# Kernel optimization log

Hardware: AMD Instinct MI355X
Metric: run time of the kernel (lower is better)

The kernel has to match this reference:

```python
import jax, jax.numpy as jnp
import numpy as np
from jax import lax

TOP_K = 2

def _unfold(x_img, k):
    # F.unfold(kernel=k, stride=k): [B,C,H,W] -> [B, C*k*k, L], column index c*k*k + kh*k + kw
    B, C, H, W = x_img.shape
    Hp, Wp = H // k, W // k
    u = x_img.reshape(B, C, Hp, k, Wp, k).transpose(0, 1, 3, 5, 2, 4)
    return u.reshape(B, C * k * k, Hp * Wp)

def _fold(p, k, H, W):
    # F.fold inverse of non-overlapping unfold: [B, C*k*k, L] -> [B,C,H,W]
    B = p.shape[0]
    C = p.shape[1] // (k * k)
    Hp, Wp = H // k, W // k
    u = p.reshape(B, C, k, k, Hp, Wp).transpose(0, 1, 4, 2, 5, 3)
    return u.reshape(B, C, H, W)

def setup_inputs() -> dict:
    key = jax.random.key(0)
    ks = jax.random.split(key, 6)
    B, H, W, C, F, E, P = 8, 64, 64, 384, 1536, 8, 4
    N = H * W
    x = jax.random.normal(ks[0], (B, N, C), dtype=jnp.float32)
    gate_w = jax.random.normal(ks[1], (E, C, P, P), dtype=jnp.float32) * 0.01
    w1 = jax.random.normal(ks[2], (E, C, F), dtype=jnp.float32) * (1.0 / np.sqrt(C))
    b1 = jax.random.normal(ks[3], (E, F), dtype=jnp.float32) * 0.01
    w2 = jax.random.normal(ks[4], (E, F, C), dtype=jnp.float32) * (1.0 / np.sqrt(F))
    b2 = jax.random.normal(ks[5], (E, C), dtype=jnp.float32) * 0.01
    return {"x": x, "gate_w": gate_w, "w1": w1, "b1": b1, "w2": w2, "b2": b2, "H": H, "W": W}

def reference(x, gate_w, w1, b1, w2, b2, H, W):
    B, N, C = x.shape
    E, _, P, _ = gate_w.shape
    k2 = P * P
    Hp, Wp = H // P, W // P
    L = Hp * Wp
    x_img = jnp.transpose(x, (0, 2, 1)).reshape(B, C, H, W)
    # router: strided conv -> logits per patch
    logits_map = lax.conv_general_dilated(
        x_img, gate_w, window_strides=(P, P), padding='VALID',
        dimension_numbers=('NCHW', 'OIHW', 'NCHW'))  # [B,E,Hp,Wp]
    router_logits = jnp.transpose(logits_map, (0, 2, 3, 1)).reshape(B, L, E)
    probs = jax.nn.softmax(router_logits, axis=-1)
    ew, ei = lax.top_k(probs, TOP_K)  # [B,L,topk]
    ew = ew / (jnp.sum(ew, axis=-1, keepdims=True) + 1e-9)
    # expand to token level (faithful to original's reshape/flatten ordering)
    ei_tok = jnp.broadcast_to(ei[:, :, None, :], (B, L, k2, TOP_K)).reshape(-1, TOP_K)
    ew_tok = jnp.broadcast_to(ew[:, :, None, :], (B, L, k2, TOP_K)).reshape(-1, TOP_K)
    # unfold + the original's (scrambled) reshape(B, C, L, k2)
    U = _unfold(x_img, P)  # [B, C*k2, L]
    x_patches = jnp.transpose(U.reshape(B, C, L, k2), (0, 2, 3, 1))  # [B,L,k2,C]
    flat_x = x_patches.reshape(-1, C)  # [T,C], T = B*L*k2
    # combine weights: zero for experts not in top-k == masked dispatch math
    cw = jnp.zeros((flat_x.shape[0], E), dtype=flat_x.dtype)
    for kk in range(TOP_K):
        cw = cw + jax.nn.one_hot(ei_tok[:, kk], E, dtype=flat_x.dtype) * ew_tok[:, kk:kk + 1]
    out = jnp.zeros_like(flat_x)
    for e in range(E):
        h = jax.nn.gelu(flat_x @ w1[e] + b1[e], approximate=False)
        y = h @ w2[e] + b2[e]
        out = out + cw[:, e:e + 1] * y
    # fold back (mirrors original's reshape/permute exactly)
    o = jnp.transpose(out.reshape(B, L, k2, C), (0, 3, 1, 2)).reshape(B, C * k2, L)
    out_img = _fold(o, P, H, W)  # [B,C,H,W]
    # original: output.transpose(1,2).reshape(B,N,C) on NCHW tensor
    output = jnp.transpose(out_img, (0, 2, 1, 3)).reshape(B, N, C)
    return output
```

## Files before the change

kernel.cpp:

```cpp
#include <hip/hip_runtime.h>
#include <hip/hip_bf16.h>

#define BB   8
#define HH   64
#define WWID 64
#define CC   384
#define FF   1536
#define EE   8
#define LL   256
#define MTOTMAX 67584
#define NTMAX   264

typedef unsigned short ushort_t;
typedef __attribute__((ext_vector_type(4))) unsigned short u16x4;
typedef __attribute__((ext_vector_type(8))) short          s16x8;
typedef __attribute__((ext_vector_type(4))) float          f32x4;

__device__ __forceinline__ float bf2f(ushort_t u) {
  union { unsigned int i; float f; } v; v.i = ((unsigned int)u) << 16; return v.f;
}
__device__ __forceinline__ ushort_t f2bf(float f) {
  union { float f; unsigned int i; } v; v.f = f;
  unsigned int u = v.i;
  u += 0x7fffu + ((u >> 16) & 1u);
  return (ushort_t)(u >> 16);
}
__device__ __forceinline__ float gelu_f(float x) {
  float x2 = x * x;
  float t  = __builtin_fmaf(x2, -0.10294325f, -2.3022082f);
  float e  = __builtin_amdgcn_exp2f(x * t);
  float r  = __builtin_amdgcn_rcpf(1.0f + e);
  return x * r;
}

#define GLDS(g, l) __builtin_amdgcn_global_load_lds( \
    (const __attribute__((address_space(1))) void*)(g), \
    (__attribute__((address_space(3))) void*)(l), 16, 0, 0)

__global__ __launch_bounds__(256) void k_transpose(const float* __restrict__ src,
                                                   ushort_t* __restrict__ dst,
                                                   int R, int Cd) {
  __shared__ ushort_t tile[32][33];
  int e  = blockIdx.z;
  int c0 = blockIdx.x * 32, r0 = blockIdx.y * 32;
  int tx = threadIdx.x & 31, ty = threadIdx.x >> 5;
  const float* s = src + (size_t)e * R * Cd;
  ushort_t*    d = dst + (size_t)e * R * Cd;
  #pragma unroll
  for (int i = 0; i < 32; i += 8)
    tile[ty + i][tx] = f2bf(s[(size_t)(r0 + ty + i) * Cd + c0 + tx]);
  __syncthreads();
  #pragma unroll
  for (int i = 0; i < 32; i += 8)
    d[(size_t)(c0 + ty + i) * R + r0 + tx] = tile[tx][ty + i];
}

__global__ void k_tgw(const float* __restrict__ gw, float* __restrict__ gwt) {
  int e = blockIdx.x, t = threadIdx.x;
  for (int i = t; i < CC * 16; i += 256) {
    int c = i >> 4, p = i & 15;
    gwt[((size_t)e * 16 + p) * CC + c] = gw[(size_t)e * CC * 16 + i];
  }
}

__global__ __launch_bounds__(256) void k_router(const float* __restrict__ x,
                                                const float* __restrict__ gwt,
                                                int* __restrict__ re, float* __restrict__ rw,
                                                int* __restrict__ cnt) {
  int bid = blockIdx.x;
  int b = bid >> 8, l2 = bid & 255;
  int hp = l2 >> 4, wp = l2 & 15;
  int t = threadIdx.x;
  int e = t >> 5, lane = t & 31;
  const float* xb = x + (size_t)b * (HH * WWID) * CC;
  const float* ge = gwt + (size_t)e * 16 * CC;
  float acc = 0.f;
  #pragma unroll
  for (int p = 0; p < 16; ++p) {
    int pix = (hp * 4 + (p >> 2)) * 64 + wp * 4 + (p & 3);
    const float* xr = xb + (size_t)pix * CC;
    const float* gr = ge + (size_t)p * CC;
    #pragma unroll
    for (int it = 0; it < 3; ++it) {
      f32x4 xv = *reinterpret_cast<const f32x4*>(xr + it * 128 + lane * 4);
      f32x4 gv = *reinterpret_cast<const f32x4*>(gr + it * 128 + lane * 4);
      acc += xv.x * gv.x + xv.y * gv.y + xv.z * gv.z + xv.w * gv.w;
    }
  }
  #pragma unroll
  for (int d = 16; d; d >>= 1) acc += __shfl_down(acc, d, 32);
  __shared__ float logits[EE];
  if (lane == 0) logits[e] = acc;
  __syncthreads();
  if (t == 0) {
    float m = logits[0];
    #pragma unroll
    for (int i = 1; i < EE; ++i) m = fmaxf(m, logits[i]);
    float p[EE]; float s = 0.f;
    #pragma unroll
    for (int i = 0; i < EE; ++i) { p[i] = __expf(logits[i] - m); s += p[i]; }
    #pragma unroll
    for (int i = 0; i < EE; ++i) p[i] /= s;
    int e0 = 0;
    #pragma unroll
    for (int i = 1; i < EE; ++i) if (p[i] > p[e0]) e0 = i;
    int e1 = (e0 == 0) ? 1 : 0;
    #pragma unroll
    for (int i = 0; i < EE; ++i) if (i != e0 && p[i] > p[e1]) e1 = i;
    float s2 = p[e0] + p[e1] + 1e-9f;
    re[bid * 2 + 0] = e0;  re[bid * 2 + 1] = e1;
    rw[bid * 2 + 0] = p[e0] / s2;  rw[bid * 2 + 1] = p[e1] / s2;
    atomicAdd(&cnt[e0], 16);
    atomicAdd(&cnt[e1], 16);
  }
}

__global__ void k_pad(const int* __restrict__ cnt, int* __restrict__ cntp,
                      int* __restrict__ basep, int* __restrict__ tile2e,
                      int* __restrict__ gids, float* __restrict__ gwts) {
  __shared__ int s_cnt[EE], s_cntp[EE], s_base[EE + 1];
  int t = threadIdx.x;
  if (t == 0) {
    int b = 0;
    for (int e = 0; e < EE; ++e) {
      int c  = cnt[e];
      int cp = (c + 255) & ~255;
      s_cnt[e] = c; s_cntp[e] = cp; s_base[e] = b;
      b += cp;
    }
    s_base[EE] = b;
  }
  __syncthreads();
  if (t < EE) { cntp[t] = s_cntp[t]; basep[t] = s_base[t]; }
  if (t == EE) basep[EE] = s_base[EE];
  int ntot = s_base[EE] >> 8;
  for (int g = t; g < ntot; g += 256) {
    int e = 0;
    #pragma unroll
    for (int i = 1; i < EE; ++i) if (g * 256 >= s_base[i]) e = i;
    tile2e[g] = e;
  }
  for (int e = 0; e < EE; ++e)
    for (int i = s_cnt[e] + t; i < s_cntp[e]; i += 256) {
      gids[s_base[e] + i] = -1;
      gwts[s_base[e] + i] = 0.f;
    }
}

__global__ void k_assign(const int* __restrict__ re, const float* __restrict__ rw,
                         const int* __restrict__ basep, int* __restrict__ cnt2,
                         int* __restrict__ gids, float* __restrict__ gwts,
                         int* __restrict__ inv) {
  int i = blockIdx.x * blockDim.x + threadIdx.x;
  if (i >= BB * LL * 2) return;
  int pat = i >> 1, slot = i & 1;
  int b = pat >> 8, l2 = pat & 255;
  int e = re[i];
  float w = rw[i];
  int t2 = l2 >> 4, hp = l2 & 15;
  int kh = t2 >> 2, kw = t2 & 3;
  int h = hp * 4 + kh;
  int row = basep[e] + atomicAdd(&cnt2[e], 16);
  #pragma unroll
  for (int j = 0; j < 16; ++j) {
    int wpix = j * 4 + kw;
    int pix = (b << 12) + (h << 6) + wpix;
    gids[row + j] = pix;
    gwts[row + j] = w;
    inv[(slot << 15) + pix] = row + j;
  }
}

__global__ __launch_bounds__(256) void k_gather(const float* __restrict__ x,
                                                const int* __restrict__ gids,
                                                const int* __restrict__ basep,
                                                ushort_t* __restrict__ Xc, int t0) {
  int g = t0 + blockIdx.x;
  if (g * 128 >= basep[EE]) return;
  __shared__ int s_id[128];
  int t = threadIdx.x;
  if (t < 128) s_id[t] = gids[g * 128 + t];
  __syncthreads();
  ushort_t* dst = Xc + (size_t)blockIdx.x * 128 * CC;
  for (int i = t; i < 128 * 96; i += 256) {
    int row = i / 96, ch = (i % 96) * 4;
    int id = s_id[row];
    f32x4 v = (f32x4){0.f, 0.f, 0.f, 0.f};
    if (id >= 0) v = *reinterpret_cast<const f32x4*>(x + (size_t)(id & 32767) * CC + ch);
    u16x4 o = {f2bf(v.x), f2bf(v.y), f2bf(v.z), f2bf(v.w)};
    *reinterpret_cast<u16x4*>(dst + (size_t)row * CC + ch) = o;
  }
}

#define STAGE(DST, KOFF)                                                      \
  { _Pragma("unroll")                                                         \
    for (int c = 0; c < NC; ++c)                                              \
      GLDS(src_c[c] + (KOFF), (DST) + (w * NC + c) * 512); }

#define PHASE(VMFULL, RD, DOST, KOFF)                                         \
  {                                                                           \
    if (VMFULL) {                                                             \
      if constexpr (NC == 4) { asm volatile("s_waitcnt vmcnt(4)" ::: "memory"); } \
      else                   { asm volatile("s_waitcnt vmcnt(3)" ::: "memory"); } \
    } else {                                                                  \
      asm volatile("s_waitcnt vmcnt(0)" ::: "memory");                        \
    }                                                                         \
    __builtin_amdgcn_s_barrier();                                             \
    __builtin_amdgcn_sched_barrier(0);                                        \
    s16x8 af[FI], bf[4];                                                      \
    _Pragma("unroll")                                                         \
    for (int i = 0; i < FI; ++i)                                              \
      af[i] = *reinterpret_cast<const s16x8*>((RD) + (wf * FI + i) * 512 + lane * 8); \
    _Pragma("unroll")                                                         \
    for (int j = 0; j < 4; ++j)                                               \
      bf[j] = *reinterpret_cast<const s16x8*>((RD) + (2 * FI + wm * 4 + j) * 512 + lane * 8); \
    asm volatile("s_waitcnt lgkmcnt(0)" ::: "memory");                        \
    __builtin_amdgcn_sched_barrier(0);                                        \
    __builtin_amdgcn_s_barrier();                                             \
    if (DOST) STAGE(RD, KOFF);                                                \
    __builtin_amdgcn_s_setprio(1);                                            \
    _Pragma("unroll")                                                         \
    for (int i = 0; i < FI; ++i)                                              \
      _Pragma("unroll")                                                       \
      for (int j = 0; j < 4; ++j)                                             \
        acc[i][j] = __builtin_amdgcn_mfma_f32_16x16x32_bf16(af[i], bf[j], acc[i][j], 0, 0, 0); \
    __builtin_amdgcn_s_setprio(0);                                            \
  }

template<int K, int NOUT, int TN, bool GELU, bool OUTG>
__global__ __launch_bounds__(512, 2) void k_gemm(const ushort_t* __restrict__ A,
                                                 const ushort_t* __restrict__ Bsrc,
                                                 const float* __restrict__ bias,
                                                 const int* __restrict__ basep,
                                                 const int* __restrict__ tile2e,
                                                 const float* __restrict__ gwts,
                                                 ushort_t* __restrict__ out, int t0) {
  constexpr int FI  = TN / 32;
  constexpr int NCH = 2 * FI + 16;
  constexpr int NC  = NCH / 8;
  constexpr int NX  = NOUT / TN;
  int nwg = NX * (int)gridDim.y;
  int wg  = (int)blockIdx.y * NX + (int)blockIdx.x;
  int id  = ((nwg & 7) == 0) ? ((wg & 7) * (nwg >> 3) + (wg >> 3)) : wg;
  int ng  = id % NX;
  int ly  = id / NX;
  int g   = t0 + ly;
  if (g * 256 >= basep[EE]) return;
  int e = tile2e[g];
  __shared__ ushort_t S[2][NCH * 512];
  int t = threadIdx.x, w = t >> 6, lane = t & 63;
  int l15 = lane & 15, q = lane >> 4;
  int wf = w & 1, wm = w >> 1;
  const ushort_t* a_src = A + ((size_t)e * NOUT + ng * TN) * K;
  const ushort_t* b_src = Bsrc + (size_t)ly * 256 * K;

  const ushort_t* src_c[NC];
  #pragma unroll
  for (int c = 0; c < NC; ++c) {
    int ch = w * NC + c;
    src_c[c] = (ch < 2 * FI)
      ? a_src + (size_t)(ch * 16 + l15) * K + q * 8
      : b_src + (size_t)((ch - 2 * FI) * 16 + l15) * K + q * 8;
  }

  f32x4 acc[FI][4];
  #pragma unroll
  for (int i = 0; i < FI; ++i)
    #pragma unroll
    for (int j = 0; j < 4; ++j) acc[i][j] = (f32x4){0.f, 0.f, 0.f, 0.f};

  ushort_t* S0 = &S[0][0];
  ushort_t* S1 = &S[1][0];

  STAGE(S0, 0);
  STAGE(S1, 32);

  constexpr int NIT = K / 32;
  for (int it = 0; it < NIT - 2; it += 2) {
    PHASE(true, S0, true, (size_t)(it + 2) * 32);
    PHASE(true, S1, true, (size_t)(it + 3) * 32);
  }
  PHASE(true,  S0, false, 0);
  PHASE(false, S1, false, 0);

  int nb = ng * TN + wf * (TN / 2) + q * 4;
  f32x4 bv[FI];
  #pragma unroll
  for (int i = 0; i < FI; ++i)
    bv[i] = *reinterpret_cast<const f32x4*>(bias + (size_t)e * NOUT + nb + i * 16);
  ushort_t* ob = out + (OUTG ? (size_t)g : (size_t)ly) * 256 * NOUT;
  #pragma unroll
  for (int j = 0; j < 4; ++j) {
    int m = wm * 64 + j * 16 + l15;
    float wt = GELU ? 1.f : gwts[g * 256 + m];
    ushort_t* op = ob + (size_t)m * NOUT + nb;
    #pragma unroll
    for (int i = 0; i < FI; ++i) {
      u16x4 v;
      #pragma unroll
      for (int r = 0; r < 4; ++r) {
        float xv = acc[i][j][r] + bv[i][r];
        v[r] = f2bf(GELU ? gelu_f(xv) : xv * wt);
      }
      *reinterpret_cast<u16x4*>(op + i * 16) = v;
    }
  }
}

__global__ __launch_bounds__(256) void k_final(const ushort_t* __restrict__ y,
                                               const int* __restrict__ inv,
                                               float* __restrict__ out) {
  int bid = blockIdx.x;
  __shared__ float tile[64][193];
  __shared__ int s_r0[64], s_r1[64];
  int t = threadIdx.x;
  if (t < 64) {
    s_r0[t] = inv[(bid << 6) + t];
    s_r1[t] = inv[32768 + (bid << 6) + t];
  }
  __syncthreads();
  float* dst = out + (size_t)bid * CC * WWID;
  #pragma unroll
  for (int half = 0; half < 2; ++half) {
    int c0 = half * 192;
    for (int i = t; i < 64 * 48; i += 256) {
      int w = i / 48, c4 = (i % 48) * 4;
      u16x4 a = *reinterpret_cast<const u16x4*>(y + (size_t)s_r0[w] * CC + c0 + c4);
      u16x4 b = *reinterpret_cast<const u16x4*>(y + (size_t)s_r1[w] * CC + c0 + c4);
      #pragma unroll
      for (int k = 0; k < 4; ++k)
        tile[w][c4 + k] = bf2f(a[k]) + bf2f(b[k]);
    }
    __syncthreads();
    for (int i = t; i < 64 * 192; i += 256) {
      int cl = i / 64, w = i % 64;
      dst[(size_t)(c0 + cl) * WWID + w] = tile[w][cl];
    }
    __syncthreads();
  }
}

extern "C" void kernel_launch(void* const* d_in, const int* in_sizes, int n_in,
                              void* d_out, int out_size, void* d_ws, size_t ws_size,
                              hipStream_t stream) {
  const float* x  = (const float*)d_in[0];
  const float* gw = (const float*)d_in[1];
  const float* w1 = (const float*)d_in[2];
  const float* b1 = (const float*)d_in[3];
  const float* w2 = (const float*)d_in[4];
  const float* b2 = (const float*)d_in[5];

  const size_t fixed = (size_t)EE * FF * CC * 2 * 2
                     + (size_t)MTOTMAX * CC * 2
                     + (size_t)EE * 16 * CC * 4
                     + (size_t)MTOTMAX * 4 * 2
                     + (size_t)65536 * 4
                     + (size_t)BB * LL * 2 * 4 * 2
                     + (size_t)NTMAX * 4
                     + 1024;
  const int cands[6] = {32768, 16384, 8192, 4096, 2048, 1024};
  int MC = 1024;
  for (int i = 0; i < 6; ++i)
    if (fixed + (size_t)cands[i] * 3840 <= ws_size) { MC = cands[i]; break; }
  const int npass = (MTOTMAX + MC - 1) / MC;
  const int nt128 = MC / 128;
  const int nt256 = MC / 256;

  char* ws = (char*)d_ws;
  size_t off = 0;
  ushort_t* Xc   = (ushort_t*)(ws + off); off += (size_t)MC * CC * 2;
  ushort_t* Hc   = (ushort_t*)(ws + off); off += (size_t)MC * FF * 2;
  ushort_t* w1t  = (ushort_t*)(ws + off); off += (size_t)EE * FF * CC * 2;
  ushort_t* w2t  = (ushort_t*)(ws + off); off += (size_t)EE * FF * CC * 2;
  ushort_t* y    = (ushort_t*)(ws + off); off += (size_t)MTOTMAX * CC * 2;
  float* gwt   = (float*)(ws + off); off += (size_t)EE * 16 * CC * 4;
  int*   gids  = (int*)(ws + off);   off += (size_t)MTOTMAX * 4;
  float* gwts  = (float*)(ws + off); off += (size_t)MTOTMAX * 4;
  int*   inv   = (int*)(ws + off);   off += (size_t)65536 * 4;
  int*   re    = (int*)(ws + off);   off += (size_t)BB * LL * 2 * 4;
  float* rw    = (float*)(ws + off); off += (size_t)BB * LL * 2 * 4;
  int*   tile2e= (int*)(ws + off);   off += (size_t)NTMAX * 4;
  int*   cnt   = (int*)(ws + off);   off += 64;
  int*   cnt2  = (int*)(ws + off);   off += 64;
  int*   cntp  = (int*)(ws + off);   off += 64;
  int*   basep = (int*)(ws + off);   off += 64;

  hipMemsetAsync(cnt, 0, 128, stream);

  k_transpose<<<dim3(FF / 32, CC / 32, EE), 256, 0, stream>>>(w1, w1t, CC, FF);
  k_transpose<<<dim3(CC / 32, FF / 32, EE), 256, 0, stream>>>(w2, w2t, FF, CC);
  k_tgw<<<EE, 256, 0, stream>>>(gw, gwt);
  k_router<<<BB * LL, 256, 0, stream>>>(x, gwt, re, rw, cnt);
  k_pad<<<1, 256, 0, stream>>>(cnt, cntp, basep, tile2e, gids, gwts);
  k_assign<<<16, 256, 0, stream>>>(re, rw, basep, cnt2, gids, gwts, inv);

  for (int p = 0; p < npass; ++p) {
    k_gather<<<nt128, 256, 0, stream>>>(x, gids, basep, Xc, p * nt128);
    k_gemm<CC, FF, 256, true,  false><<<dim3(FF / 256, nt256), 512, 0, stream>>>(
        w1t, Xc, b1, basep, tile2e, (const float*)nullptr, Hc, p * nt256);
    k_gemm<FF, CC, 128, false, true ><<<dim3(CC / 128, nt256), 512, 0, stream>>>(
        w2t, Hc, b2, basep, tile2e, gwts, y, p * nt256);
  }
  k_final<<<BB * HH, 256, 0, stream>>>(y, inv, (float*)d_out);
}
```

Before: 655.1 us.

## Switch MoE GEMMs to 192x192 tiles with 4 waves and triple-buffered LDS

Both expert GEMMs move from 256-row tiles (256xTN with 8 waves) to 192x192 tiles computed by 4 waves. Each wave now holds a 6x6 MFMA accumulator block, and a three-stage LDS ring replaces the double buffer. Expert token padding drops from multiples of 256 to multiples of 192, which cuts wasted padded rows, and the larger per-wave tile raises MFMA work per LDS read. The cost is heavy register pressure from 36 f32x4 accumulators, 72KB of dynamic LDS per block, and the loss of the XCD-swizzle divisibility for some grid shapes. Pass chunk sizes and workspace constants are rescaled to match.

Measured after the change: 592.9 us. -9.5%, faster.

```diff
diff --git a/kernel.cpp b/kernel.cpp
--- a/kernel.cpp
+++ b/kernel.cpp
@@ -8,8 +8,8 @@
 #define FF   1536
 #define EE   8
 #define LL   256
-#define MTOTMAX 67584
-#define NTMAX   264
+#define MTOTMAX 67200
+#define NTMAX   352
 
 typedef unsigned short ushort_t;
 typedef __attribute__((ext_vector_type(4))) unsigned short u16x4;
@@ -124,7 +124,7 @@
     int b = 0;
     for (int e = 0; e < EE; ++e) {
       int c  = cnt[e];
-      int cp = (c + 255) & ~255;
+      int cp = ((c + 191) / 192) * 192;
       s_cnt[e] = c; s_cntp[e] = cp; s_base[e] = b;
       b += cp;
     }
@@ -133,11 +133,11 @@
   __syncthreads();
   if (t < EE) { cntp[t] = s_cntp[t]; basep[t] = s_base[t]; }
   if (t == EE) basep[EE] = s_base[EE];
-  int ntot = s_base[EE] >> 8;
+  int ntot = s_base[EE] / 192;
   for (int g = t; g < ntot; g += 256) {
     int e = 0;
     #pragma unroll
-    for (int i = 1; i < EE; ++i) if (g * 256 >= s_base[i]) e = i;
+    for (int i = 1; i < EE; ++i) if (g * 192 >= s_base[i]) e = i;
     tile2e[g] = e;
   }
   for (int e = 0; e < EE; ++e)
@@ -194,108 +194,104 @@
 
 #define STAGE(DST, KOFF)                                                      \
   { _Pragma("unroll")                                                         \
-    for (int c = 0; c < NC; ++c)                                              \
-      GLDS(src_c[c] + (KOFF), (DST) + (w * NC + c) * 512); }
-
-#define PHASE(VMFULL, RD, DOST, KOFF)                                         \
+    for (int c = 0; c < 6; ++c)                                               \
+      GLDS(src_c[c] + (KOFF), (DST) + (w * 6 + c) * 512); }
+
+#define PHASE(VM, RD, DOST, KOFF)                                             \
   {                                                                           \
-    if (VMFULL) {                                                             \
-      if constexpr (NC == 4) { asm volatile("s_waitcnt vmcnt(4)" ::: "memory"); } \
-      else                   { asm volatile("s_waitcnt vmcnt(3)" ::: "memory"); } \
-    } else {                                                                  \
-      asm volatile("s_waitcnt vmcnt(0)" ::: "memory");                        \
-    }                                                                         \
+    asm volatile("s_waitcnt vmcnt(" VM ")" ::: "memory");                     \
     __builtin_amdgcn_s_barrier();                                             \
     __builtin_amdgcn_sched_barrier(0);                                        \
-    s16x8 af[FI], bf[4];                                                      \
+    s16x8 af[6], bf[6];                                                       \
     _Pragma("unroll")                                                         \
-    for (int i = 0; i < FI; ++i)                                              \
-      af[i] = *reinterpret_cast<const s16x8*>((RD) + (wf * FI + i) * 512 + lane * 8); \
+    for (int i = 0; i < 6; ++i)                                               \
+      af[i] = *reinterpret_cast<const s16x8*>((RD) + (wf * 6 + i) * 512 + lane * 8); \
     _Pragma("unroll")                                                         \
-    for (int j = 0; j < 4; ++j)                                               \
-      bf[j] = *reinterpret_cast<const s16x8*>((RD) + (2 * FI + wm * 4 + j) * 512 + lane * 8); \
+    for (int j = 0; j < 6; ++j)                                               \
+      bf[j] = *reinterpret_cast<const s16x8*>((RD) + (12 + wm * 6 + j) * 512 + lane * 8); \
     asm volatile("s_waitcnt lgkmcnt(0)" ::: "memory");                        \
     __builtin_amdgcn_sched_barrier(0);                                        \
     __builtin_amdgcn_s_barrier();                                             \
     if (DOST) STAGE(RD, KOFF);                                                \
     __builtin_amdgcn_s_setprio(1);                                            \
     _Pragma("unroll")                                                         \
-    for (int i = 0; i < FI; ++i)                                              \
+    for (int i = 0; i < 6; ++i)                                               \
       _Pragma("unroll")                                                       \
-      for (int j = 0; j < 4; ++j)                                             \
+      for (int j = 0; j < 6; ++j)                                             \
         acc[i][j] = __builtin_amdgcn_mfma_f32_16x16x32_bf16(af[i], bf[j], acc[i][j], 0, 0, 0); \
     __builtin_amdgcn_s_setprio(0);                                            \
   }
 
-template<int K, int NOUT, int TN, bool GELU, bool OUTG>
-__global__ __launch_bounds__(512, 2) void k_gemm(const ushort_t* __restrict__ A,
+template<int K, int NOUT, bool GELU, bool OUTG>
+__global__ __launch_bounds__(256, 2) void k_gemm(const ushort_t* __restrict__ A,
                                                  const ushort_t* __restrict__ Bsrc,
                                                  const float* __restrict__ bias,
                                                  const int* __restrict__ basep,
                                                  const int* __restrict__ tile2e,
                                                  const float* __restrict__ gwts,
                                                  ushort_t* __restrict__ out, int t0) {
-  constexpr int FI  = TN / 32;
-  constexpr int NCH = 2 * FI + 16;
-  constexpr int NC  = NCH / 8;
-  constexpr int NX  = NOUT / TN;
+  constexpr int NX = NOUT / 192;
+  extern __shared__ ushort_t S[];
   int nwg = NX * (int)gridDim.y;
   int wg  = (int)blockIdx.y * NX + (int)blockIdx.x;
   int id  = ((nwg & 7) == 0) ? ((wg & 7) * (nwg >> 3) + (wg >> 3)) : wg;
   int ng  = id % NX;
   int ly  = id / NX;
   int g   = t0 + ly;
-  if (g * 256 >= basep[EE]) return;
+  if (g * 192 >= basep[EE]) return;
   int e = tile2e[g];
-  __shared__ ushort_t S[2][NCH * 512];
   int t = threadIdx.x, w = t >> 6, lane = t & 63;
   int l15 = lane & 15, q = lane >> 4;
   int wf = w & 1, wm = w >> 1;
-  const ushort_t* a_src = A + ((size_t)e * NOUT + ng * TN) * K;
-  const ushort_t* b_src = Bsrc + (size_t)ly * 256 * K;
-
-  const ushort_t* src_c[NC];
-  #pragma unroll
-  for (int c = 0; c < NC; ++c) {
-    int ch = w * NC + c;
-    src_c[c] = (ch < 2 * FI)
+  const ushort_t* a_src = A + ((size_t)e * NOUT + ng * 192) * K;
+  const ushort_t* b_src = Bsrc + (size_t)ly * 192 * K;
+
+  const ushort_t* src_c[6];
+  #pragma unroll
+  for (int c = 0; c < 6; ++c) {
+    int ch = w * 6 + c;
+    src_c[c] = (ch < 12)
       ? a_src + (size_t)(ch * 16 + l15) * K + q * 8
-      : b_src + (size_t)((ch - 2 * FI) * 16 + l15) * K + q * 8;
-  }
-
-  f32x4 acc[FI][4];
-  #pragma unroll
-  for (int i = 0; i < FI; ++i)
-    #pragma unroll
-    for (int j = 0; j < 4; ++j) acc[i][j] = (f32x4){0.f, 0.f, 0.f, 0.f};
-
-  ushort_t* S0 = &S[0][0];
-  ushort_t* S1 = &S[1][0];
+      : b_src + (size_t)((ch - 12) * 16 + l15) * K + q * 8;
+  }
+
+  f32x4 acc[6][6];
+  #pragma unroll
+  for (int i = 0; i < 6; ++i)
+    #pragma unroll
+    for (int j = 0; j < 6; ++j) acc[i][j] = (f32x4){0.f, 0.f, 0.f, 0.f};
+
+  ushort_t* S0 = S;
+  ushort_t* S1 = S + 12288;
+  ushort_t* S2 = S + 24576;
 
   STAGE(S0, 0);
   STAGE(S1, 32);
+  STAGE(S2, 64);
 
   constexpr int NIT = K / 32;
-  for (int it = 0; it < NIT - 2; it += 2) {
-    PHASE(true, S0, true, (size_t)(it + 2) * 32);
-    PHASE(true, S1, true, (size_t)(it + 3) * 32);
-  }
-  PHASE(true,  S0, false, 0);
-  PHASE(false, S1, false, 0);
-
-  int nb = ng * TN + wf * (TN / 2) + q * 4;
-  f32x4 bv[FI];
-  #pragma unroll
-  for (int i = 0; i < FI; ++i)
+  for (int it = 0; it < NIT - 3; it += 3) {
+    PHASE("12", S0, true, (size_t)(it + 3) * 32);
+    PHASE("12", S1, true, (size_t)(it + 4) * 32);
+    PHASE("12", S2, true, (size_t)(it + 5) * 32);
+  }
+  PHASE("12", S0, false, 0);
+  PHASE("6",  S1, false, 0);
+  PHASE("0",  S2, false, 0);
+
+  int nb = ng * 192 + wf * 96 + q * 4;
+  f32x4 bv[6];
+  #pragma unroll
+  for (int i = 0; i < 6; ++i)
     bv[i] = *reinterpret_cast<const f32x4*>(bias + (size_t)e * NOUT + nb + i * 16);
-  ushort_t* ob = out + (OUTG ? (size_t)g : (size_t)ly) * 256 * NOUT;
-  #pragma unroll
-  for (int j = 0; j < 4; ++j) {
-    int m = wm * 64 + j * 16 + l15;
-    float wt = GELU ? 1.f : gwts[g * 256 + m];
+  ushort_t* ob = out + (size_t)(OUTG ? g : ly) * 192 * NOUT;
+  #pragma unroll
+  for (int j = 0; j < 6; ++j) {
+    int m = wm * 96 + j * 16 + l15;
+    float wt = GELU ? 1.f : gwts[g * 192 + m];
     ushort_t* op = ob + (size_t)m * NOUT + nb;
     #pragma unroll
-    for (int i = 0; i < FI; ++i) {
+    for (int i = 0; i < 6; ++i) {
       u16x4 v;
       #pragma unroll
       for (int r = 0; r < 4; ++r) {
@@ -350,21 +346,21 @@
   const float* w2 = (const float*)d_in[4];
   const float* b2 = (const float*)d_in[5];
 
-  const size_t fixed = (size_t)EE * FF * CC * 2 * 2
-                     + (size_t)MTOTMAX * CC * 2
-                     + (size_t)EE * 16 * CC * 4
-                     + (size_t)MTOTMAX * 4 * 2
-                     + (size_t)65536 * 4
-                     + (size_t)BB * LL * 2 * 4 * 2
-                     + (size_t)NTMAX * 4
-                     + 1024;
-  const int cands[6] = {32768, 16384, 8192, 4096, 2048, 1024};
-  int MC = 1024;
-  for (int i = 0; i < 6; ++i)
-    if (fixed + (size_t)cands[i] * 3840 <= ws_size) { MC = cands[i]; break; }
+  const size_t fixed2 = (size_t)EE * FF * CC * 2 * 2
+                      + (size_t)MTOTMAX * CC * 2
+                      + (size_t)EE * 16 * CC * 4
+                      + (size_t)MTOTMAX * 4 * 2
+                      + (size_t)65536 * 4
+                      + (size_t)BB * LL * 2 * 4 * 2
+                      + (size_t)NTMAX * 4
+                      + 1024;
+  const int cands[4] = {33792, 16896, 8448, 4224};
+  int MC = 4224;
+  for (int i = 0; i < 4; ++i)
+    if (fixed2 + (size_t)cands[i] * 3840 <= ws_size) { MC = cands[i]; break; }
   const int npass = (MTOTMAX + MC - 1) / MC;
   const int nt128 = MC / 128;
-  const int nt256 = MC / 256;
+  const int ntg   = MC / 192;
 
   char* ws = (char*)d_ws;
   size_t off = 0;
@@ -394,12 +390,13 @@
   k_pad<<<1, 256, 0, stream>>>(cnt, cntp, basep, tile2e, gids, gwts);
   k_assign<<<16, 256, 0, stream>>>(re, rw, basep, cnt2, gids, gwts, inv);
 
+  const int shmem = 3 * 24 * 1024;
   for (int p = 0; p < npass; ++p) {
     k_gather<<<nt128, 256, 0, stream>>>(x, gids, basep, Xc, p * nt128);
-    k_gemm<CC, FF, 256, true,  false><<<dim3(FF / 256, nt256), 512, 0, stream>>>(
-        w1t, Xc, b1, basep, tile2e, (const float*)nullptr, Hc, p * nt256);
-    k_gemm<FF, CC, 128, false, true ><<<dim3(CC / 128, nt256), 512, 0, stream>>>(
-        w2t, Hc, b2, basep, tile2e, gwts, y, p * nt256);
+    k_gemm<CC, FF, true,  false><<<dim3(FF / 192, ntg), 256, shmem, stream>>>(
+        w1t, Xc, b1, basep, tile2e, (const float*)nullptr, Hc, p * ntg);
+    k_gemm<FF, CC, false, true ><<<dim3(CC / 192, ntg), 256, shmem, stream>>>(
+        w2t, Hc, b2, basep, tile2e, gwts, y, p * ntg);
   }
   k_final<<<BB * HH, 256, 0, stream>>>(y, inv, (float*)d_out);
 }
```
